# Kernel tuning notes

Measured on AMD Instinct MI355X. Metric: run time of the kernel, lower is better.

The kernel has to match this reference:

```python
import jax, jax.numpy as jnp
import numpy as np

DIM = 768
NUM_HEADS = 12
HEAD_DIM = DIM // NUM_HEADS
SCALE = HEAD_DIM ** (-0.5)
WH, WW = 14, 14
NUM_EXTRA = 1
NUM_REL_DIST = (2 * WH - 1) * (2 * WW - 1) + NUM_EXTRA * (NUM_EXTRA + 2)  # 732
N_TOK = WH * WW + NUM_EXTRA  # 197
BATCH = 64


def make_rel_pos_index():
    # mirrors the torch buffer construction (meshgrid 'ij')
    coords = np.stack(np.meshgrid(np.arange(WH), np.arange(WW), indexing='ij'))  # [2,Wh,Ww]
    coords_flat = coords.reshape(2, -1)  # [2, Wh*Ww]
    rel = coords_flat[:, :, None] - coords_flat[:, None, :]  # [2, M, M]
    rel = rel.transpose(1, 2, 0).astype(np.int64)  # [M, M, 2]
    rel[:, :, 0] += WH - 1
    rel[:, :, 1] += WW - 1
    rel[:, :, 0] *= 2 * WW - 1
    idx = np.zeros((N_TOK, N_TOK), dtype=np.int64)
    idx[NUM_EXTRA:, NUM_EXTRA:] = rel.sum(-1)
    idx[0, 0:] = NUM_REL_DIST - 3
    idx[0:, 0] = NUM_REL_DIST - 2
    idx[0, 0] = NUM_REL_DIST - 1
    return jnp.asarray(idx, dtype=jnp.int32)


def setup_inputs() -> dict:
    key = jax.random.key(0)
    ks = jax.random.split(key, 7)
    x = jax.random.normal(ks[0], (BATCH, N_TOK, DIM), dtype=jnp.float32)
    qkv_w = jax.random.normal(ks[1], (3 * DIM, DIM), dtype=jnp.float32) * (DIM ** -0.5)
    q_bias = jax.random.normal(ks[2], (DIM,), dtype=jnp.float32) * 0.02
    v_bias = jax.random.normal(ks[3], (DIM,), dtype=jnp.float32) * 0.02
    rpb_table = jax.random.normal(ks[4], (NUM_REL_DIST, NUM_HEADS), dtype=jnp.float32) * 0.02
    proj_w = jax.random.normal(ks[5], (DIM, DIM), dtype=jnp.float32) * (DIM ** -0.5)
    proj_b = jax.random.normal(ks[6], (DIM,), dtype=jnp.float32) * 0.02
    rel_index = make_rel_pos_index()
    return {"x": x, "qkv_w": qkv_w, "q_bias": q_bias, "v_bias": v_bias,
            "rpb_table": rpb_table, "proj_w": proj_w, "proj_b": proj_b,
            "rel_index": rel_index}


def reference(x, qkv_w, q_bias, v_bias, rpb_table, proj_w, proj_b, rel_index):
    B, N, C = x.shape
    # qkv bias: [q_bias, zeros, v_bias]
    qkv_bias = jnp.concatenate([q_bias, jnp.zeros_like(v_bias), v_bias]).astype(x.dtype)
    qkv = x @ qkv_w.T + qkv_bias  # [B,N,3C]
    qkv = qkv.reshape(B, N, 3, NUM_HEADS, HEAD_DIM).transpose(2, 0, 3, 1, 4)  # [3,B,H,N,d]
    q, k, v = qkv[0] * SCALE, qkv[1], qkv[2]
    # fp32 scores, as in the original
    attn = jnp.einsum('bhnd,bhmd->bhnm', q.astype(jnp.float32), k.astype(jnp.float32))
    # relative position bias gather: [N,N,H] -> [H,N,N]
    bias = rpb_table[rel_index.reshape(-1)].reshape(N, N, NUM_HEADS).transpose(2, 0, 1)
    attn = jax.nn.softmax(attn + bias[None].astype(jnp.float32), axis=-1)
    out = jnp.einsum('bhnm,bhmd->bhnd', attn, v.astype(attn.dtype))
    out = out.transpose(0, 2, 1, 3).reshape(B, N, -1).astype(x.dtype)
    return out @ proj_w.T + proj_b
```

## Files before the change

### kernel.cpp

```cpp
#include <hip/hip_runtime.h>
#include <hip/hip_bf16.h>

#define DIM 768
#define NHEADS 12
#define HD 64
#define NTOK 197
#define BATCH 64
#define NTOKENS (BATCH*NTOK)
#define NPAIR (NTOK*NTOK)
#define QK_SCALE 0.125f
#define CDIM 2304

typedef short bf16x8 __attribute__((ext_vector_type(8)));
typedef float f32x4 __attribute__((ext_vector_type(4)));

#define MFMA(a,b,c) __builtin_amdgcn_mfma_f32_16x16x32_bf16(a,b,c,0,0,0)

__device__ __forceinline__ unsigned short f2bf(float f) {
    union { float f; unsigned u; } v; v.f = f;
    unsigned r = v.u + 0x7FFFu + ((v.u >> 16) & 1u);
    return (unsigned short)(r >> 16);
}

__device__ __forceinline__ void gload16(const unsigned short* g, unsigned short* l) {
    __builtin_amdgcn_global_load_lds(
        (const __attribute__((address_space(1))) void*)g,
        (__attribute__((address_space(3))) void*)l, 16, 0, 0);
}

__device__ __forceinline__ int xcd_swz(int orig, int nwg) {
    int q = nwg >> 3, r = nwg & 7;
    int xcd = orig & 7, idx = orig >> 3;
    return (xcd < r ? xcd * (q + 1) : r * (q + 1) + (xcd - r) * q) + idx;
}

#define NB_X 4728
#define NB_WQ 864
#define NB_WP 288
#define NB_BIAS 1820

__device__ __forceinline__ void cvt8(const float* __restrict__ s,
                                     unsigned short* __restrict__ d, int t, int n8) {
    if (t >= n8) return;
    float4 a = ((const float4*)s)[t * 2], b = ((const float4*)s)[t * 2 + 1];
    union { unsigned short u[8]; bf16x8 v; } p;
    p.u[0] = f2bf(a.x); p.u[1] = f2bf(a.y); p.u[2] = f2bf(a.z); p.u[3] = f2bf(a.w);
    p.u[4] = f2bf(b.x); p.u[5] = f2bf(b.y); p.u[6] = f2bf(b.z); p.u[7] = f2bf(b.w);
    ((bf16x8*)d)[t] = p.v;
}

__global__ __launch_bounds__(256) void prep(
    const float* __restrict__ x, const float* __restrict__ qw,
    const float* __restrict__ pw, const float* __restrict__ rpb,
    const int* __restrict__ rel,
    unsigned short* __restrict__ Xb, unsigned short* __restrict__ Wqb,
    unsigned short* __restrict__ Wpb, float* __restrict__ biasm)
{
    int bid = blockIdx.x;
    if (bid < NB_X) {
        cvt8(x, Xb, bid * 256 + threadIdx.x, NB_X * 256);
    } else if (bid < NB_X + NB_WQ) {
        cvt8(qw, Wqb, (bid - NB_X) * 256 + threadIdx.x, NB_WQ * 256);
    } else if (bid < NB_X + NB_WQ + NB_WP) {
        cvt8(pw, Wpb, (bid - NB_X - NB_WQ) * 256 + threadIdx.x, NB_WP * 256);
    } else {
        int t = (bid - NB_X - NB_WQ - NB_WP) * 256 + threadIdx.x;
        if (t < NHEADS * NPAIR) {
            int h = t / NPAIR, p = t - h * NPAIR;
            biasm[t] = rpb[rel[p] * NHEADS + h];
        }
    }
}

#define NKT 12
#define BUFE 16384

__global__ __launch_bounds__(512, 2) void gemm_qkv8(
    const unsigned short* __restrict__ Xb, const unsigned short* __restrict__ Wb,
    const float* __restrict__ qbias, const float* __restrict__ vbias,
    unsigned short* __restrict__ QKVb)
{
    __shared__ __attribute__((aligned(16))) unsigned short AsF[2 * BUFE];
    __shared__ __attribute__((aligned(16))) unsigned short BsF[2 * BUFE];
    int tid = threadIdx.x, lane = tid & 63, wid = tid >> 6;
    int wr = wid >> 2, wc = wid & 3;
    int wg = xcd_swz(blockIdx.x, 450);
    int bx = wg / 9, by = wg % 9;
    int m0 = bx * 256, n0 = by * 256;
    int r15 = lane & 15, hi = lane >> 4, sx = lane & 7;
    int sl0 = hi ^ sx, sl1 = (hi + 4) ^ sx;

    size_t asrc[4], bsrc[4];
    int adoff[4];
    #pragma unroll
    for (int i = 0; i < 4; ++i) {
        int c = i * 512 + tid;
        int row = c >> 3, s = c & 7, rr = row & 127, half = row >> 7;
        int slot = s ^ (rr & 7);
        int ar = m0 + row; if (ar >= NTOKENS) ar = NTOKENS - 1;
        asrc[i] = (size_t)ar * DIM + slot * 8;
        bsrc[i] = (size_t)(n0 + row) * DIM + slot * 8;
        adoff[i] = half * 8192 + rr * 64 + s * 8;
    }
    int abase0 = wr * 8192 + r15 * 64;
    int bbase0 = (wc >> 1) * 8192 + (wc & 1) * 4096 + r15 * 64;

    f32x4 acc[8][4];
    #pragma unroll
    for (int i = 0; i < 8; ++i)
        #pragma unroll
        for (int j = 0; j < 4; ++j) acc[i][j] = (f32x4){0.f, 0.f, 0.f, 0.f};

#define STAGE(buf, kt) do { \
    _Pragma("unroll") \
    for (int i = 0; i < 4; ++i) { \
        gload16(Xb + asrc[i] + (kt) * 64, &AsF[(buf) * BUFE + adoff[i]]); \
        gload16(Wb + bsrc[i] + (kt) * 64, &BsF[(buf) * BUFE + adoff[i]]); \
    } } while (0)

    bf16x8 af[4][2], bw[2][2];
#define PHASE(mh, nh, LA, LB, bo) do { \
    if (LA) { _Pragma("unroll") for (int mi = 0; mi < 4; ++mi) { \
        af[mi][0] = *(const bf16x8*)&AsF[(bo) + abase0 + ((mh)*4+mi)*1024 + sl0*8]; \
        af[mi][1] = *(const bf16x8*)&AsF[(bo) + abase0 + ((mh)*4+mi)*1024 + sl1*8]; } } \
    if (LB) { _Pragma("unroll") for (int ni = 0; ni < 2; ++ni) { \
        bw[ni][0] = *(const bf16x8*)&BsF[(bo) + bbase0 + ((nh)*2+ni)*1024 + sl0*8]; \
        bw[ni][1] = *(const bf16x8*)&BsF[(bo) + bbase0 + ((nh)*2+ni)*1024 + sl1*8]; } } \
    __builtin_amdgcn_s_setprio(1); \
    _Pragma("unroll") for (int mi = 0; mi < 4; ++mi) \
        _Pragma("unroll") for (int ni = 0; ni < 2; ++ni) { \
            acc[(mh)*4+mi][(nh)*2+ni] = MFMA(af[mi][0], bw[ni][0], acc[(mh)*4+mi][(nh)*2+ni]); \
            acc[(mh)*4+mi][(nh)*2+ni] = MFMA(af[mi][1], bw[ni][1], acc[(mh)*4+mi][(nh)*2+ni]); } \
    __builtin_amdgcn_s_setprio(0); \
} while (0)

    STAGE(0, 0);
    STAGE(1, 1);
    asm volatile("s_waitcnt vmcnt(8)" ::: "memory");
    __builtin_amdgcn_s_barrier();

    for (int t = 0; t < NKT; ++t) {
        int bo = (t & 1) * BUFE;
        PHASE(0, 0, 1, 1, bo);
        PHASE(0, 1, 0, 1, bo);
        PHASE(1, 1, 1, 0, bo);
        PHASE(1, 0, 0, 1, bo);
        __builtin_amdgcn_s_barrier();
        if (t + 2 < NKT) {
            STAGE(t & 1, t + 2);
            asm volatile("s_waitcnt vmcnt(8)" ::: "memory");
        } else {
            asm volatile("s_waitcnt vmcnt(0)" ::: "memory");
        }
        __builtin_amdgcn_s_barrier();
    }

    unsigned short* reg = (wid < 4) ? &AsF[wid * 8192] : &BsF[(wid - 4) * 8192];
    {
        int which = n0 / DIM;
        float scl = (which == 0) ? QK_SCALE : 1.f;
        #pragma unroll
        for (int n = 0; n < 4; ++n) {
            int colr = n0 - which * DIM + wc * 64 + n * 16 + r15;
            float bv = (which == 0) ? qbias[colr] : (which == 2 ? vbias[colr] : 0.f);
            #pragma unroll
            for (int m = 0; m < 8; ++m) {
                int lrb = m * 16 + hi * 4;
                #pragma unroll
                for (int r = 0; r < 4; ++r) {
                    int lr = lrb + r;
                    int c = n * 16 + r15;
                    reg[lr * 64 + (c ^ (((lr >> 2) & 3) << 4))] =
                        f2bf((acc[m][n][r] + bv) * scl);
                }
            }
        }
    }
    #pragma unroll
    for (int it = 0; it < 16; ++it) {
        int c = it * 64 + lane;
        int lr = c >> 3, cc = c & 7;
        int row = m0 + wr * 128 + lr;
        if (row < NTOKENS) {
            bf16x8 v = *(bf16x8*)&reg[lr * 64 + ((cc * 8) ^ (((lr >> 2) & 3) << 4))];
            *(bf16x8*)(QKVb + (size_t)row * CDIM + n0 + wc * 64 + cc * 8) = v;
        }
    }
#undef STAGE
#undef PHASE
}

__global__ __launch_bounds__(512, 2) void gemm_proj8(
    const unsigned short* __restrict__ Ob, const unsigned short* __restrict__ Wp,
    const float* __restrict__ pbias, float* __restrict__ out)
{
    __shared__ __attribute__((aligned(16))) unsigned short AsF[2 * BUFE];
    __shared__ __attribute__((aligned(16))) unsigned short BsF[2 * BUFE];
    int tid = threadIdx.x, lane = tid & 63, wid = tid >> 6;
    int wr = wid >> 2, wc = wid & 3;
    int wg = xcd_swz(blockIdx.x, 150);
    int bx = wg / 3, by = wg % 3;
    int m0 = bx * 256, n0 = by * 256;
    int r15 = lane & 15, hi = lane >> 4, sx = lane & 7;
    int sl0 = hi ^ sx, sl1 = (hi + 4) ^ sx;

    size_t asrc[4], bsrc[4];
    int adoff[4];
    #pragma unroll
    for (int i = 0; i < 4; ++i) {
        int c = i * 512 + tid;
        int row = c >> 3, s = c & 7, rr = row & 127, half = row >> 7;
        int slot = s ^ (rr & 7);
        int ar = m0 + row; if (ar >= NTOKENS) ar = NTOKENS - 1;
        asrc[i] = (size_t)ar * DIM + slot * 8;
        bsrc[i] = (size_t)(n0 + row) * DIM + slot * 8;
        adoff[i] = half * 8192 + rr * 64 + s * 8;
    }
    int abase0 = wr * 8192 + r15 * 64;
    int bbase0 = (wc >> 1) * 8192 + (wc & 1) * 4096 + r15 * 64;

    f32x4 acc[8][4];
    #pragma unroll
    for (int i = 0; i < 8; ++i)
        #pragma unroll
        for (int j = 0; j < 4; ++j) acc[i][j] = (f32x4){0.f, 0.f, 0.f, 0.f};

#define STAGE(buf, kt) do { \
    _Pragma("unroll") \
    for (int i = 0; i < 4; ++i) { \
        gload16(Ob + asrc[i] + (kt) * 64, &AsF[(buf) * BUFE + adoff[i]]); \
        gload16(Wp + bsrc[i] + (kt) * 64, &BsF[(buf) * BUFE + adoff[i]]); \
    } } while (0)

    bf16x8 af[4][2], bw[2][2];
#define PHASE(mh, nh, LA, LB, bo) do { \
    if (LA) { _Pragma("unroll") for (int mi = 0; mi < 4; ++mi) { \
        af[mi][0] = *(const bf16x8*)&AsF[(bo) + abase0 + ((mh)*4+mi)*1024 + sl0*8]; \
        af[mi][1] = *(const bf16x8*)&AsF[(bo) + abase0 + ((mh)*4+mi)*1024 + sl1*8]; } } \
    if (LB) { _Pragma("unroll") for (int ni = 0; ni < 2; ++ni) { \
        bw[ni][0] = *(const bf16x8*)&BsF[(bo) + bbase0 + ((nh)*2+ni)*1024 + sl0*8]; \
        bw[ni][1] = *(const bf16x8*)&BsF[(bo) + bbase0 + ((nh)*2+ni)*1024 + sl1*8]; } } \
    __builtin_amdgcn_s_setprio(1); \
    _Pragma("unroll") for (int mi = 0; mi < 4; ++mi) \
        _Pragma("unroll") for (int ni = 0; ni < 2; ++ni) { \
            acc[(mh)*4+mi][(nh)*2+ni] = MFMA(af[mi][0], bw[ni][0], acc[(mh)*4+mi][(nh)*2+ni]); \
            acc[(mh)*4+mi][(nh)*2+ni] = MFMA(af[mi][1], bw[ni][1], acc[(mh)*4+mi][(nh)*2+ni]); } \
    __builtin_amdgcn_s_setprio(0); \
} while (0)

    STAGE(0, 0);
    STAGE(1, 1);
    asm volatile("s_waitcnt vmcnt(8)" ::: "memory");
    __builtin_amdgcn_s_barrier();

    for (int t = 0; t < NKT; ++t) {
        int bo = (t & 1) * BUFE;
        PHASE(0, 0, 1, 1, bo);
        PHASE(0, 1, 0, 1, bo);
        PHASE(1, 1, 1, 0, bo);
        PHASE(1, 0, 0, 1, bo);
        __builtin_amdgcn_s_barrier();
        if (t + 2 < NKT) {
            STAGE(t & 1, t + 2);
            asm volatile("s_waitcnt vmcnt(8)" ::: "memory");
        } else {
            asm volatile("s_waitcnt vmcnt(0)" ::: "memory");
        }
        __builtin_amdgcn_s_barrier();
    }
#undef STAGE
#undef PHASE

    #pragma unroll
    for (int n = 0; n < 4; ++n) {
        int col = n0 + wc * 64 + n * 16 + r15;
        float bv = pbias[col];
        #pragma unroll
        for (int m = 0; m < 8; ++m) {
            #pragma unroll
            for (int r = 0; r < 4; ++r) {
                int row = m0 + wr * 128 + m * 16 + hi * 4 + r;
                if (row < NTOKENS)
                    out[(size_t)row * DIM + col] = acc[m][n][r] + bv;
            }
        }
    }
}

#define KP 72
#define PP 232
#define VPITCH 256

__global__ __launch_bounds__(256, 2) void attn(
    const unsigned short* __restrict__ QKV, const float* __restrict__ biasm,
    unsigned short* __restrict__ O)
{
    __shared__ __attribute__((aligned(16))) unsigned short VT[64 * VPITCH];
    __shared__ __attribute__((aligned(16))) unsigned short KlPl[208 * KP];

    int tid = threadIdx.x, lane = tid & 63, wid = tid >> 6;
    int r15 = lane & 15, hi = lane >> 4;
    int wg = blockIdx.x;
    int g = wg >> 5, qt = (wg >> 3) & 3, p = wg & 7;
    int bh = g * 8 + p;
    int h = bh % NHEADS, b = bh / NHEADS;
    size_t tb = (size_t)b * NTOK;
    int hq = h * 64;
    int rbase = qt * 64 + wid * 16 + hi * 4;

    int kcol = (tid & 7) * 8;
    bf16x8 kreg[7];
    #pragma unroll
    for (int t = 0; t < 7; ++t) {
        int row = t * 32 + (tid >> 3);
        int rc = row < NTOK ? row : (NTOK - 1);
        kreg[t] = *(const bf16x8*)(QKV + (tb + rc) * CDIM + 768 + hq + kcol);
    }
    #pragma unroll
    for (int t = 0; t < 7; ++t) {
        int row = t * 32 + (tid >> 3);
        if (row < NTOK)
            *(bf16x8*)&KlPl[row * KP + kcol] = kreg[t];
    }

    bf16x8 v0r[4], v1r[4];
    #pragma unroll
    for (int it = 0; it < 4; ++it) {
        int c = it * 256 + tid;
        int rp = c >> 3, kc = c & 7;
        int r0 = 2 * rp, r1 = 2 * rp + 1;
        bf16x8 z = (bf16x8)(short)0;
        v0r[it] = z; v1r[it] = z;
        if (r0 < NTOK) v0r[it] = *(const bf16x8*)(QKV + (tb + r0) * CDIM + 1536 + hq + kc * 8);
        if (r1 < NTOK) v1r[it] = *(const bf16x8*)(QKV + (tb + r1) * CDIM + 1536 + hq + kc * 8);
    }

    int qrow_g = qt * 64 + wid * 16 + r15;
    int qsrc = qrow_g < NTOK ? qrow_g : (NTOK - 1);
    bf16x8 aq[2];
    #pragma unroll
    for (int ks = 0; ks < 2; ++ks)
        aq[ks] = *(const bf16x8*)(QKV + (tb + qsrc) * CDIM + hq + ks * 32 + hi * 8);

    float breg[4][13];
    {
        const float* bb = biasm + h * NPAIR;
        #pragma unroll
        for (int r = 0; r < 4; ++r) {
            int row_g = rbase + r;
            int rowc = row_g < NTOK ? row_g : (NTOK - 1);
            const float* brow = bb + rowc * NTOK + r15;
            #pragma unroll
            for (int t = 0; t < 13; ++t) {
                int off = t * 16;
                if (t == 12 && r15 >= 5) off = 0;
                breg[r][t] = brow[off];
            }
        }
    }
    __syncthreads();

    f32x4 sa[13];
    #pragma unroll
    for (int t = 0; t < 13; ++t) sa[t] = (f32x4){0.f,0.f,0.f,0.f};
    __builtin_amdgcn_s_setprio(1);
    #pragma unroll
    for (int t = 0; t < 13; ++t) {
        #pragma unroll
        for (int ks = 0; ks < 2; ++ks) {
            bf16x8 bk = *(bf16x8*)&KlPl[(t * 16 + r15) * KP + ks * 32 + hi * 8];
            sa[t] = MFMA(aq[ks], bk, sa[t]);
        }
    }
    __builtin_amdgcn_s_setprio(0);
    __syncthreads();

    #pragma unroll
    for (int it = 0; it < 4; ++it) {
        int c = it * 256 + tid;
        int rp = c >> 3, kc = c & 7;
        if (rp < 112) {
            #pragma unroll
            for (int j = 0; j < 8; ++j) {
                unsigned int w = (unsigned int)(unsigned short)v0r[it][j] |
                                 ((unsigned int)(unsigned short)v1r[it][j] << 16);
                int slot2 = (rp >> 2) ^ j ^ kc;
                *(unsigned int*)&VT[(kc * 8 + j) * VPITCH + slot2 * 8 + (rp & 3) * 2] = w;
            }
        }
    }

    int plbase = wid * (16 * PP);
    float invr[4];
    #pragma unroll
    for (int r = 0; r < 4; ++r) {
        #pragma unroll
        for (int t = 0; t < 13; ++t) {
            int col = t * 16 + r15;
            if (col < NTOK) sa[t][r] += breg[r][t];
            else            sa[t][r] = -1e30f;
        }
        float mx = sa[0][r];
        #pragma unroll
        for (int t = 1; t < 13; ++t) mx = fmaxf(mx, sa[t][r]);
        #pragma unroll
        for (int m = 1; m < 16; m <<= 1) mx = fmaxf(mx, __shfl_xor(mx, m));
        float sum = 0.f;
        #pragma unroll
        for (int t = 0; t < 13; ++t) {
            float e = __expf(sa[t][r] - mx);
            sa[t][r] = e; sum += e;
        }
        int roff = plbase + (hi * 4 + r) * PP;
        #pragma unroll
        for (int t = 0; t < 13; ++t)
            KlPl[roff + t * 16 + r15] = f2bf(sa[t][r]);
        KlPl[roff + 208 + r15] = 0;
        #pragma unroll
        for (int m = 1; m < 16; m <<= 1) sum += __shfl_xor(sum, m);
        invr[r] = __builtin_amdgcn_rcpf(sum);
    }
    __syncthreads();

    f32x4 oa[4];
    #pragma unroll
    for (int dt = 0; dt < 4; ++dt) oa[dt] = (f32x4){0.f,0.f,0.f,0.f};
    int X = hi ^ (r15 & 7) ^ (r15 >> 3);
    __builtin_amdgcn_s_setprio(1);
    #pragma unroll
    for (int ks = 0; ks < 7; ++ks) {
        bf16x8 ap = *(bf16x8*)&KlPl[plbase + r15 * PP + ks * 32 + hi * 8];
        #pragma unroll
        for (int dt = 0; dt < 4; ++dt) {
            int d = dt * 16 + r15;
            int slotp = (ks * 4) ^ (dt * 2) ^ X;
            bf16x8 bv = *(bf16x8*)&VT[d * VPITCH + slotp * 8];
            oa[dt] = MFMA(ap, bv, oa[dt]);
        }
    }
    __builtin_amdgcn_s_setprio(0);

    #pragma unroll
    for (int dt = 0; dt < 4; ++dt)
        #pragma unroll
        for (int r = 0; r < 4; ++r)
            KlPl[plbase + (hi * 4 + r) * 72 + dt * 16 + r15] = f2bf(oa[dt][r] * invr[r]);
    #pragma unroll
    for (int it = 0; it < 2; ++it) {
        int c = it * 64 + lane;
        int lr = c >> 3, cc = c & 7;
        int qrow = qt * 64 + wid * 16 + lr;
        if (qrow < NTOK)
            *(bf16x8*)(O + (tb + qrow) * DIM + hq + cc * 8) =
                *(bf16x8*)&KlPl[plbase + lr * 72 + cc * 8];
    }
}

extern "C" void kernel_launch(void* const* d_in, const int* in_sizes, int n_in,
                              void* d_out, int out_size, void* d_ws, size_t ws_size,
                              hipStream_t stream) {
    const float* x      = (const float*)d_in[0];
    const float* qkv_w  = (const float*)d_in[1];
    const float* q_bias = (const float*)d_in[2];
    const float* v_bias = (const float*)d_in[3];
    const float* rpb    = (const float*)d_in[4];
    const float* proj_w = (const float*)d_in[5];
    const float* proj_b = (const float*)d_in[6];
    const int*   rel    = (const int*)d_in[7];
    float* out = (float*)d_out;

    const size_t NELEM = (size_t)NTOKENS * DIM;
    const size_t WQKV  = (size_t)3 * DIM * DIM;
    const size_t WPROJ = (size_t)DIM * DIM;
    unsigned short* Xb   = (unsigned short*)d_ws;
    unsigned short* Wqb  = Xb + NELEM;
    unsigned short* Wpb  = Wqb + WQKV;
    unsigned short* QKVb = Wpb + WPROJ;
    float* biasm = (float*)(QKVb + (size_t)NTOKENS * CDIM);
    unsigned short* Ob = Xb;

    prep<<<NB_X + NB_WQ + NB_WP + NB_BIAS, 256, 0, stream>>>(
        x, qkv_w, proj_w, rpb, rel, Xb, Wqb, Wpb, biasm);

    gemm_qkv8<<<450, 512, 0, stream>>>(Xb, Wqb, q_bias, v_bias, QKVb);

    attn<<<3072, 256, 0, stream>>>(QKVb, biasm, Ob);

    gemm_proj8<<<150, 512, 0, stream>>>(Ob, Wpb, proj_b, out);
}
```

Before: 165.5 us.

## Interleave global prefetch with MFMA phases using 8-wave ping-pong schedule in GEMMs

Replaces the two-tile-ahead prefetch loop in the QKV and projection GEMMs with a one-tile-ahead double-buffered schedule. The next tile's global-to-LDS loads are split into quarter chunks issued between MFMA phases, with a barrier around each phase. The goal is to spread memory traffic across compute and keep LDS reads and MFMAs overlapped in a ping-pong style. The cost is many more barriers per k-tile and only one tile of prefetch distance, so more load latency may be exposed.

```diff
diff --git a/kernel.cpp b/kernel.cpp
--- a/kernel.cpp
+++ b/kernel.cpp
@@ -73,7 +73,46 @@
 }
 
 #define NKT 12
+#define TMAX 6
 #define BUFE 16384
+
+#define LDA(bo, mh) do { _Pragma("unroll") for (int mi = 0; mi < 4; ++mi) { \
+    af[mi][0] = *(const bf16x8*)&AsF[(bo) + abase0 + ((mh)*4+mi)*1024 + sl0*8]; \
+    af[mi][1] = *(const bf16x8*)&AsF[(bo) + abase0 + ((mh)*4+mi)*1024 + sl1*8]; } } while(0)
+#define LDB(bo, nh) do { _Pragma("unroll") for (int ni = 0; ni < 2; ++ni) { \
+    bw[ni][0] = *(const bf16x8*)&BsF[(bo) + bbase0 + ((nh)*2+ni)*1024 + sl0*8]; \
+    bw[ni][1] = *(const bf16x8*)&BsF[(bo) + bbase0 + ((nh)*2+ni)*1024 + sl1*8]; } } while(0)
+#define MM(mh, nh) do { __builtin_amdgcn_s_setprio(1); \
+    _Pragma("unroll") for (int mi = 0; mi < 4; ++mi) \
+    _Pragma("unroll") for (int ni = 0; ni < 2; ++ni) { \
+        acc[(mh)*4+mi][(nh)*2+ni] = MFMA(af[mi][0], bw[ni][0], acc[(mh)*4+mi][(nh)*2+ni]); \
+        acc[(mh)*4+mi][(nh)*2+ni] = MFMA(af[mi][1], bw[ni][1], acc[(mh)*4+mi][(nh)*2+ni]); } \
+    __builtin_amdgcn_s_setprio(0); } while(0)
+#define SA(Ap, buf, h, kt) do { \
+    gload16(Ap + asrc[2*(h)] + (kt)*64, &AsF[(buf)*BUFE + adoff[2*(h)]]); \
+    gload16(Ap + asrc[2*(h)+1] + (kt)*64, &AsF[(buf)*BUFE + adoff[2*(h)+1]]); } while(0)
+#define SB(Bp, buf, h, kt) do { \
+    gload16(Bp + bsrc[2*(h)] + (kt)*64, &BsF[(buf)*BUFE + adoff[2*(h)]]); \
+    gload16(Bp + bsrc[2*(h)+1] + (kt)*64, &BsF[(buf)*BUFE + adoff[2*(h)+1]]); } while(0)
+#define BAR __builtin_amdgcn_s_barrier()
+#define WVM0 asm volatile("s_waitcnt vmcnt(0)" ::: "memory")
+
+#define KLOOP(Ap, Bp) \
+    SA(Ap, 0, 0, 0); SA(Ap, 0, 1, 0); SB(Bp, 0, 0, 0); SB(Bp, 0, 1, 0); \
+    WVM0; BAR; \
+    for (int t = 0; t < TMAX; ++t) { \
+        int k1 = 2 * t + 1, k2 = 2 * t + 2; \
+        bool st = (t < TMAX - 1); \
+        LDA(0, 0); LDB(0, 0); SA(Ap, 1, 0, k1);            BAR; MM(0, 0); BAR; \
+        LDB(0, 1);            SA(Ap, 1, 1, k1);            BAR; MM(0, 1); BAR; \
+        LDA(0, 1);            SB(Bp, 1, 0, k1);            BAR; MM(1, 1); BAR; \
+        LDB(0, 0);            SB(Bp, 1, 1, k1);            BAR; MM(1, 0); WVM0; BAR; \
+        LDA(BUFE, 0); LDB(BUFE, 0); if (st) SA(Ap, 0, 0, k2); BAR; MM(0, 0); BAR; \
+        LDB(BUFE, 1);               if (st) SA(Ap, 0, 1, k2); BAR; MM(0, 1); BAR; \
+        LDA(BUFE, 1);               if (st) SB(Bp, 0, 0, k2); BAR; MM(1, 1); BAR; \
+        LDB(BUFE, 0);               if (st) SB(Bp, 0, 1, k2); BAR; MM(1, 0); \
+        if (st) { WVM0; } BAR; \
+    }
 
 __global__ __launch_bounds__(512, 2) void gemm_qkv8(
     const unsigned short* __restrict__ Xb, const unsigned short* __restrict__ Wb,
@@ -111,49 +150,8 @@
         #pragma unroll
         for (int j = 0; j < 4; ++j) acc[i][j] = (f32x4){0.f, 0.f, 0.f, 0.f};
 
-#define STAGE(buf, kt) do { \
-    _Pragma("unroll") \
-    for (int i = 0; i < 4; ++i) { \
-        gload16(Xb + asrc[i] + (kt) * 64, &AsF[(buf) * BUFE + adoff[i]]); \
-        gload16(Wb + bsrc[i] + (kt) * 64, &BsF[(buf) * BUFE + adoff[i]]); \
-    } } while (0)
-
     bf16x8 af[4][2], bw[2][2];
-#define PHASE(mh, nh, LA, LB, bo) do { \
-    if (LA) { _Pragma("unroll") for (int mi = 0; mi < 4; ++mi) { \
-        af[mi][0] = *(const bf16x8*)&AsF[(bo) + abase0 + ((mh)*4+mi)*1024 + sl0*8]; \
-        af[mi][1] = *(const bf16x8*)&AsF[(bo) + abase0 + ((mh)*4+mi)*1024 + sl1*8]; } } \
-    if (LB) { _Pragma("unroll") for (int ni = 0; ni < 2; ++ni) { \
-        bw[ni][0] = *(const bf16x8*)&BsF[(bo) + bbase0 + ((nh)*2+ni)*1024 + sl0*8]; \
-        bw[ni][1] = *(const bf16x8*)&BsF[(bo) + bbase0 + ((nh)*2+ni)*1024 + sl1*8]; } } \
-    __builtin_amdgcn_s_setprio(1); \
-    _Pragma("unroll") for (int mi = 0; mi < 4; ++mi) \
-        _Pragma("unroll") for (int ni = 0; ni < 2; ++ni) { \
-            acc[(mh)*4+mi][(nh)*2+ni] = MFMA(af[mi][0], bw[ni][0], acc[(mh)*4+mi][(nh)*2+ni]); \
-            acc[(mh)*4+mi][(nh)*2+ni] = MFMA(af[mi][1], bw[ni][1], acc[(mh)*4+mi][(nh)*2+ni]); } \
-    __builtin_amdgcn_s_setprio(0); \
-} while (0)
-
-    STAGE(0, 0);
-    STAGE(1, 1);
-    asm volatile("s_waitcnt vmcnt(8)" ::: "memory");
-    __builtin_amdgcn_s_barrier();
-
-    for (int t = 0; t < NKT; ++t) {
-        int bo = (t & 1) * BUFE;
-        PHASE(0, 0, 1, 1, bo);
-        PHASE(0, 1, 0, 1, bo);
-        PHASE(1, 1, 1, 0, bo);
-        PHASE(1, 0, 0, 1, bo);
-        __builtin_amdgcn_s_barrier();
-        if (t + 2 < NKT) {
-            STAGE(t & 1, t + 2);
-            asm volatile("s_waitcnt vmcnt(8)" ::: "memory");
-        } else {
-            asm volatile("s_waitcnt vmcnt(0)" ::: "memory");
-        }
-        __builtin_amdgcn_s_barrier();
-    }
+    KLOOP(Xb, Wb)
 
     unsigned short* reg = (wid < 4) ? &AsF[wid * 8192] : &BsF[(wid - 4) * 8192];
     {
@@ -186,8 +184,6 @@
             *(bf16x8*)(QKVb + (size_t)row * CDIM + n0 + wc * 64 + cc * 8) = v;
         }
     }
-#undef STAGE
-#undef PHASE
 }
 
 __global__ __launch_bounds__(512, 2) void gemm_proj8(
@@ -225,51 +221,8 @@
         #pragma unroll
         for (int j = 0; j < 4; ++j) acc[i][j] = (f32x4){0.f, 0.f, 0.f, 0.f};
 
-#define STAGE(buf, kt) do { \
-    _Pragma("unroll") \
-    for (int i = 0; i < 4; ++i) { \
-        gload16(Ob + asrc[i] + (kt) * 64, &AsF[(buf) * BUFE + adoff[i]]); \
-        gload16(Wp + bsrc[i] + (kt) * 64, &BsF[(buf) * BUFE + adoff[i]]); \
-    } } while (0)
-
     bf16x8 af[4][2], bw[2][2];
-#define PHASE(mh, nh, LA, LB, bo) do { \
-    if (LA) { _Pragma("unroll") for (int mi = 0; mi < 4; ++mi) { \
-        af[mi][0] = *(const bf16x8*)&AsF[(bo) + abase0 + ((mh)*4+mi)*1024 + sl0*8]; \
-        af[mi][1] = *(const bf16x8*)&AsF[(bo) + abase0 + ((mh)*4+mi)*1024 + sl1*8]; } } \
-    if (LB) { _Pragma("unroll") for (int ni = 0; ni < 2; ++ni) { \
-        bw[ni][0] = *(const bf16x8*)&BsF[(bo) + bbase0 + ((nh)*2+ni)*1024 + sl0*8]; \
-        bw[ni][1] = *(const bf16x8*)&BsF[(bo) + bbase0 + ((nh)*2+ni)*1024 + sl1*8]; } } \
-    __builtin_amdgcn_s_setprio(1); \
-    _Pragma("unroll") for (int mi = 0; mi < 4; ++mi) \
-        _Pragma("unroll") for (int ni = 0; ni < 2; ++ni) { \
-            acc[(mh)*4+mi][(nh)*2+ni] = MFMA(af[mi][0], bw[ni][0], acc[(mh)*4+mi][(nh)*2+ni]); \
-            acc[(mh)*4+mi][(nh)*2+ni] = MFMA(af[mi][1], bw[ni][1], acc[(mh)*4+mi][(nh)*2+ni]); } \
-    __builtin_amdgcn_s_setprio(0); \
-} while (0)
-
-    STAGE(0, 0);
-    STAGE(1, 1);
-    asm volatile("s_waitcnt vmcnt(8)" ::: "memory");
-    __builtin_amdgcn_s_barrier();
-
-    for (int t = 0; t < NKT; ++t) {
-        int bo = (t & 1) * BUFE;
-        PHASE(0, 0, 1, 1, bo);
-        PHASE(0, 1, 0, 1, bo);
-        PHASE(1, 1, 1, 0, bo);
-        PHASE(1, 0, 0, 1, bo);
-        __builtin_amdgcn_s_barrier();
-        if (t + 2 < NKT) {
-            STAGE(t & 1, t + 2);
-            asm volatile("s_waitcnt vmcnt(8)" ::: "memory");
-        } else {
-            asm volatile("s_waitcnt vmcnt(0)" ::: "memory");
-        }
-        __builtin_amdgcn_s_barrier();
-    }
-#undef STAGE
-#undef PHASE
+    KLOOP(Ob, Wp)
 
     #pragma unroll
     for (int n = 0; n < 4; ++n) {
```

New measurement: 166.3 us. About the same (+0.4%).
